# Kernel tuning notes

Measured on AMD Instinct MI355X. Metric: run time of the kernel, lower is better.

Reference implementation:

```python
import jax, jax.numpy as jnp
import numpy as np

EPS = 1e-05
NEG = -1e9

def rotate_half(x):
    x1, x2 = jnp.split(x, 2, axis=-1)
    return jnp.concatenate([-x2, x1], axis=-1)

def rmsnorm(x, w):
    xf = x.astype(jnp.float32)
    n = xf * jax.lax.rsqrt(jnp.mean(xf * xf, axis=-1, keepdims=True) + EPS)
    return w * n.astype(x.dtype)

def setup_inputs() -> dict:
    key = jax.random.key(0)
    ks = jax.random.split(key, 12)
    B, S, H, NH, DH, FF = 1, 2048, 2048, 16, 128, 8192
    x = jax.random.normal(ks[0], (B, S, H), jnp.float32)
    # additive causal mask [1,1,S,S]
    causal = jnp.where(jnp.tril(jnp.ones((S, S), bool)), 0.0, NEG).astype(jnp.float32)
    attention_mask = causal[None, None]
    alibi = 0.1 * jax.random.normal(ks[1], (1, NH, S, S), jnp.float32)
    # rotary angles [S, DH]
    inv = 1.0 / (10000.0 ** (jnp.arange(0, DH, 2, dtype=jnp.float32) / DH))
    ang = jnp.arange(S, dtype=jnp.float32)[:, None] * inv[None, :]
    freqs = jnp.concatenate([ang, ang], axis=-1)  # [S, DH]
    sc = 1.0 / np.sqrt(H)
    wq = sc * jax.random.normal(ks[2], (H, H), jnp.float32)
    wk = sc * jax.random.normal(ks[3], (H, H), jnp.float32)
    wv = sc * jax.random.normal(ks[4], (H, H), jnp.float32)
    wo = sc * jax.random.normal(ks[5], (H, H), jnp.float32)
    w1 = sc * jax.random.normal(ks[6], (H, FF), jnp.float32)
    w3 = sc * jax.random.normal(ks[7], (H, FF), jnp.float32)
    w2 = (1.0 / np.sqrt(FF)) * jax.random.normal(ks[8], (FF, H), jnp.float32)
    attn_norm_w = jnp.ones((H,), jnp.float32)
    ffn_norm_w = jnp.ones((H,), jnp.float32)
    return dict(x=x, attention_mask=attention_mask, alibi=alibi, freqs=freqs,
                wq=wq, wk=wk, wv=wv, wo=wo, w1=w1, w2=w2, w3=w3,
                attn_norm_w=attn_norm_w, ffn_norm_w=ffn_norm_w)

def reference(x, attention_mask, alibi, freqs, wq, wk, wv, wo, w1, w2, w3,
              attn_norm_w, ffn_norm_w):
    B, S, H = x.shape
    NH = 16
    DH = H // NH
    nx = rmsnorm(x, attn_norm_w)
    # projections -> [B, NH, S, DH]
    def heads(y):
        return y.reshape(B, S, NH, DH).transpose(0, 2, 1, 3)
    q = heads(nx @ wq)
    k = heads(nx @ wk)
    v = heads(nx @ wv)
    cos, sin = jnp.cos(freqs), jnp.sin(freqs)  # [S, DH] broadcasts over B,NH
    q = q * cos + rotate_half(q) * sin
    k = k * cos + rotate_half(k) * sin
    scores = jnp.einsum('bhqd,bhkd->bhqk', q, k) / np.sqrt(DH)
    scores = scores + attention_mask + alibi
    attn = jax.nn.softmax(scores, axis=-1)
    out = jnp.einsum('bhqk,bhkd->bhqd', attn, v)
    out = out.transpose(0, 2, 1, 3).reshape(B, S, H)
    x = x + out @ wo
    nx = rmsnorm(x, ffn_norm_w)
    ff = (jax.nn.silu(nx @ w1) * (nx @ w3)) @ w2
    return x + ff
```

## Files before the change

### kernel.cpp

```cpp
#include <hip/hip_runtime.h>
#include <hip/hip_bf16.h>
#include <math.h>

typedef __bf16 bf16x8 __attribute__((ext_vector_type(8)));
typedef float  f32x4  __attribute__((ext_vector_type(4)));
typedef unsigned short u16x8 __attribute__((ext_vector_type(8)));
typedef unsigned short u16x4 __attribute__((ext_vector_type(4)));

#define DEV static __device__ __forceinline__

DEV void gload16(const void* g, void* l) {
  __builtin_amdgcn_global_load_lds((__attribute__((address_space(1))) void*)g,
                                   (__attribute__((address_space(3))) void*)l,
                                   16, 0, 0);
}

DEV float bf2f(unsigned short u) {
  unsigned v = ((unsigned)u) << 16;
  return __builtin_bit_cast(float, v);
}
DEV unsigned short f2bf(float f) {
  unsigned u = __builtin_bit_cast(unsigned, f);
  u = u + 0x7fffu + ((u >> 16) & 1u);
  return (unsigned short)(u >> 16);
}

__global__ __launch_bounds__(256) void rmsnorm_k(const float* __restrict__ x,
    const float* __restrict__ w, unsigned short* __restrict__ out, int H) {
  int row = blockIdx.x;
  const float4* xr = (const float4*)(x + (size_t)row * H);
  float4 a = xr[threadIdx.x * 2], b = xr[threadIdx.x * 2 + 1];
  float ss = a.x*a.x + a.y*a.y + a.z*a.z + a.w*a.w
           + b.x*b.x + b.y*b.y + b.z*b.z + b.w*b.w;
#pragma unroll
  for (int o = 32; o; o >>= 1) ss += __shfl_down(ss, o, 64);
  __shared__ float red[4];
  if ((threadIdx.x & 63) == 0) red[threadIdx.x >> 6] = ss;
  __syncthreads();
  float rs = rsqrtf((red[0] + red[1] + red[2] + red[3]) * (1.0f / 2048.0f) + 1e-5f);
  size_t base = (size_t)row * H + threadIdx.x * 8;
  const float* wv = w + threadIdx.x * 8;
  float vals[8] = {a.x, a.y, a.z, a.w, b.x, b.y, b.z, b.w};
  u16x8 o8;
#pragma unroll
  for (int i = 0; i < 8; ++i) o8[i] = f2bf(vals[i] * rs * wv[i]);
  *(u16x8*)(out + base) = o8;
}

DEV void wtrans_body(const float* __restrict__ W, unsigned short* __restrict__ Wt,
                     int R, int C, int ilv, int bx, int by, int t,
                     unsigned short (*tile)[68]) {
  const int c0 = bx * 64, r0 = by * 64;
  const int lr = t >> 4, lc4 = (t & 15) * 4;
#pragma unroll
  for (int i = 0; i < 4; ++i) {
    float4 v = *(const float4*)&W[(size_t)(r0 + lr + i * 16) * C + c0 + lc4];
    u16x4 s4;
    s4[0] = f2bf(v.x); s4[1] = f2bf(v.y); s4[2] = f2bf(v.z); s4[3] = f2bf(v.w);
    *(u16x4*)&tile[lr + i * 16][lc4] = s4;
  }
  __syncthreads();
  const int oc = t >> 3, seg = (t & 7) * 8;
#pragma unroll
  for (int i = 0; i < 2; ++i) {
    int c = c0 + oc + i * 32;
    u16x8 o8;
#pragma unroll
    for (int j = 0; j < 8; ++j) o8[j] = tile[seg + j][oc + i * 32];
    size_t dstrow = (ilv < 0) ? (size_t)c
                              : (size_t)(c >> 4) * 32 + (c & 15) + ilv * 16;
    *(u16x8*)&Wt[dstrow * R + r0 + seg] = o8;
  }
}

__global__ __launch_bounds__(256) void wtrans64_k(const float* __restrict__ W,
    unsigned short* __restrict__ Wt, int R, int C, int ilv) {
  __shared__ unsigned short tile[64][68];
  wtrans_body(W, Wt, R, C, ilv, blockIdx.x, blockIdx.y, threadIdx.x, tile);
}

__global__ __launch_bounds__(256) void wtrans4_k(
    const float* __restrict__ s0, const float* __restrict__ s1,
    const float* __restrict__ s2, const float* __restrict__ s3,
    unsigned short* __restrict__ d0, unsigned short* __restrict__ d1,
    unsigned short* __restrict__ d2, unsigned short* __restrict__ d3,
    int R, int C) {
  __shared__ unsigned short tile[64][68];
  const float* s = (blockIdx.z == 0) ? s0 : (blockIdx.z == 1) ? s1
                 : (blockIdx.z == 2) ? s2 : s3;
  unsigned short* d = (blockIdx.z == 0) ? d0 : (blockIdx.z == 1) ? d1
                    : (blockIdx.z == 2) ? d2 : d3;
  wtrans_body(s, d, R, C, -1, blockIdx.x, blockIdx.y, threadIdx.x, tile);
}

__global__ __launch_bounds__(256) void wtrans13_k(
    const float* __restrict__ w1, const float* __restrict__ w3,
    unsigned short* __restrict__ dst, int R, int C) {
  __shared__ unsigned short tile[64][68];
  const float* s = blockIdx.z ? w3 : w1;
  wtrans_body(s, dst, R, C, (int)blockIdx.z, blockIdx.x, blockIdx.y,
              threadIdx.x, tile);
}

#define STG_A(H, BUF, KC) do {                                                 \
    gload16(Asrc0 + (size_t)(H) * 128 * lda + (KC),                            \
            &lds[(BUF) * 16384 + (H) * 8192 + w * 1024]);                      \
    gload16(Asrc1 + (size_t)(H) * 128 * lda + (KC),                            \
            &lds[(BUF) * 16384 + (H) * 8192 + w * 1024 + 512]);                \
  } while (0)

#define STG_B(H, BUF, KC) do {                                                 \
    gload16(Bsrc0 + (size_t)(H) * 128 * ldb + (KC),                            \
            &lds[32768 + (BUF) * 16384 + (H) * 8192 + w * 1024]);              \
    gload16(Bsrc1 + (size_t)(H) * 128 * ldb + (KC),                            \
            &lds[32768 + (BUF) * 16384 + (H) * 8192 + w * 1024 + 512]);        \
  } while (0)

#define DS_A(DST, MH) do {                                                     \
    const int abase = buf * 16384 + (MH) * 8192 + arow * 64;                   \
    _Pragma("unroll") for (int m = 0; m < 4; ++m) {                            \
      DST[m][0] = *(const bf16x8*)&lds[abase + m * 1024 + acol0];              \
      DST[m][1] = *(const bf16x8*)&lds[abase + m * 1024 + acol1];              \
    } } while (0)

#define DS_B(DST, NH) do {                                                     \
    const int bbase = 32768 + buf * 16384 + (NH) * 8192 + brow * 64;           \
    _Pragma("unroll") for (int n = 0; n < 2; ++n) {                            \
      DST[n][0] = *(const bf16x8*)&lds[bbase + n * 1024 + acol0];              \
      DST[n][1] = *(const bf16x8*)&lds[bbase + n * 1024 + acol1];              \
    } } while (0)

#define MFMA16(AI, AR, BR) do {                                                \
    _Pragma("unroll") for (int m = 0; m < 4; ++m)                              \
      _Pragma("unroll") for (int n = 0; n < 2; ++n) {                          \
        acc[AI][m][n] = __builtin_amdgcn_mfma_f32_16x16x32_bf16(               \
            AR[m][0], BR[n][0], acc[AI][m][n], 0, 0, 0);                       \
        acc[AI][m][n] = __builtin_amdgcn_mfma_f32_16x16x32_bf16(               \
            AR[m][1], BR[n][1], acc[AI][m][n], 0, 0, 0);                       \
      }                                                                        \
  } while (0)

template <int EPI>
__global__ __launch_bounds__(512, 2) void gemm256_k(
    const unsigned short* __restrict__ A, int lda,
    const unsigned short* __restrict__ B, int ldb,
    unsigned short* __restrict__ Cb, float* __restrict__ Cf,
    int M, int N, int Kext) {
  __shared__ unsigned short lds[65536];
  const int t = threadIdx.x, w = t >> 6, lane = t & 63;
  const int nbm = M >> 8, nbn = N >> 8, nwg = nbm * nbn;
  int id = blockIdx.x;
  id = (id & 7) * (nwg >> 3) + (id >> 3);
  const int bm = id % nbm, bn = id / nbm;
  const size_t m0 = (size_t)bm << 8, n0 = (size_t)bn << 8;
  const int koff = blockIdx.y * Kext;
  const int NT = Kext >> 6;
  const int scol = ((lane & 7) ^ (lane >> 3)) * 8;
  const unsigned short* Asrc0 = A + (m0 + w * 16 + (lane >> 3)) * (size_t)lda + koff + scol;
  const unsigned short* Asrc1 = A + (m0 + w * 16 + 8 + (lane >> 3)) * (size_t)lda + koff + scol;
  const unsigned short* Bsrc0 = B + (n0 + w * 16 + (lane >> 3)) * (size_t)ldb + koff + scol;
  const unsigned short* Bsrc1 = B + (n0 + w * 16 + 8 + (lane >> 3)) * (size_t)ldb + koff + scol;
  const int arow = (w >> 2) * 64 + (lane & 15);
  const int brow = (w & 3) * 32 + (lane & 15);
  const int acol0 = ((lane >> 4) * 8) ^ ((lane & 7) << 3);
  const int acol1 = acol0 ^ 32;
  f32x4 acc[4][4][2] = {};
  bf16x8 Acur[4][2], B0r[2][2], B1r[2][2];
  STG_A(0, 0, 0); STG_B(0, 0, 0); STG_A(1, 0, 0); STG_B(1, 0, 0);
  STG_A(0, 1, 64); STG_B(0, 1, 64);
  asm volatile("s_waitcnt vmcnt(4)" ::: "memory");
  __builtin_amdgcn_s_barrier();
  for (int kt = 0; kt < NT; ++kt) {
    const int buf = kt & 1;
    const int kc1 = (kt + 1) * 64, kc2 = (kt + 2) * 64;
    const bool p1 = (kt + 1 < NT), p2 = (kt + 2 < NT);
    DS_A(Acur, 0); DS_B(B0r, 0); DS_B(B1r, 1);
    if (p1) { STG_A(1, buf ^ 1, kc1); STG_B(1, buf ^ 1, kc1); }
    __builtin_amdgcn_sched_barrier(0);
    __builtin_amdgcn_s_barrier();
    __builtin_amdgcn_s_setprio(1);
    MFMA16(0, Acur, B0r);
    MFMA16(1, Acur, B1r);
    __builtin_amdgcn_s_setprio(0);
    __builtin_amdgcn_sched_barrier(0);
    __builtin_amdgcn_s_barrier();
    DS_A(Acur, 1);
    if (p2) { STG_A(0, buf, kc2); STG_B(0, buf, kc2); }
    __builtin_amdgcn_sched_barrier(0);
    __builtin_amdgcn_s_barrier();
    __builtin_amdgcn_s_setprio(1);
    MFMA16(2, Acur, B0r);
    MFMA16(3, Acur, B1r);
    __builtin_amdgcn_s_setprio(0);
    __builtin_amdgcn_sched_barrier(0);
    if (p2) { asm volatile("s_waitcnt vmcnt(4)" ::: "memory"); }
    else    { asm volatile("s_waitcnt vmcnt(0)" ::: "memory"); }
    __builtin_amdgcn_s_barrier();
  }
#pragma unroll
  for (int Mh = 0; Mh < 2; ++Mh)
#pragma unroll
    for (int Nh = 0; Nh < 2; ++Nh)
#pragma unroll
      for (int m = 0; m < 4; ++m) {
        size_t gr = m0 + Mh * 128 + (w >> 2) * 64 + m * 16 + (lane >> 4) * 4;
        if constexpr (EPI == 2) {
          size_t gc = (n0 >> 1) + Nh * 64 + (w & 3) * 16 + (lane & 15);
          f32x4 v0 = acc[Mh * 2 + Nh][m][0];
          f32x4 v1 = acc[Mh * 2 + Nh][m][1];
#pragma unroll
          for (int j = 0; j < 4; ++j) {
            float s = v0[j] / (1.0f + __expf(-v0[j]));
            Cb[(gr + j) * (size_t)(N >> 1) + gc] = f2bf(s * v1[j]);
          }
        } else {
#pragma unroll
          for (int n = 0; n < 2; ++n) {
            size_t gc = n0 + Nh * 128 + (w & 3) * 32 + n * 16 + (lane & 15);
            f32x4 v = acc[Mh * 2 + Nh][m][n];
#pragma unroll
            for (int j = 0; j < 4; ++j) {
              size_t o = (gr + j) * (size_t)N + gc;
              if constexpr (EPI == 0) Cb[o] = f2bf(v[j]);
              else Cf[(size_t)blockIdx.y * M * N + o] = v[j];
            }
          }
        }
      }
}

template <int EPI>
__global__ __launch_bounds__(256) void gemm_bt_k(
    const unsigned short* __restrict__ A, const unsigned short* __restrict__ B,
    float* __restrict__ Cf, unsigned short* __restrict__ Cb,
    const float* __restrict__ resid, int M, int N, int K) {
  constexpr int BK = 64;
  __shared__ unsigned short lA[128 * BK];
  __shared__ unsigned short lB[128 * BK];
  const int t = threadIdx.x, wave = t >> 6, lane = t & 63;
  int nwg = gridDim.x * gridDim.y;
  int id = blockIdx.y * gridDim.x + blockIdx.x;
  id = (id & 7) * (nwg >> 3) + (id >> 3);
  const int m0 = (id % gridDim.x) * 128, n0 = (id / gridDim.x) * 128;
  const int wr = (wave >> 1) * 64, wc = (wave & 1) * 64;
  f32x4 acc[4][4] = {};
  const int sr = t >> 3;
  const int sc = ((t & 7) ^ (sr & 7)) * 8;
  const unsigned short* Ab = A + (size_t)(m0 + sr) * K + sc;
  const unsigned short* Bb = B + (size_t)(n0 + sr) * K + sc;
  unsigned short* lAw = &lA[(wave * 8) * BK];
  unsigned short* lBw = &lB[(wave * 8) * BK];
  const int row = lane & 15, kg = (lane >> 4) * 8, swz = (lane & 7) << 3;
  for (int k0 = 0; k0 < K; k0 += BK) {
#pragma unroll
    for (int it = 0; it < 4; ++it) {
      gload16(Ab + (size_t)it * 32 * K + k0, lAw + it * 32 * BK);
      gload16(Bb + (size_t)it * 32 * K + k0, lBw + it * 32 * BK);
    }
    asm volatile("s_waitcnt vmcnt(0)" ::: "memory");
    __syncthreads();
#pragma unroll
    for (int kk = 0; kk < 2; ++kk) {
      bf16x8 af[4], bfr[4];
#pragma unroll
      for (int m = 0; m < 4; ++m)
        af[m] = *(const bf16x8*)&lA[(wr + m * 16 + row) * BK + ((kk * 32 + kg) ^ swz)];
#pragma unroll
      for (int n = 0; n < 4; ++n)
        bfr[n] = *(const bf16x8*)&lB[(wc + n * 16 + row) * BK + ((kk * 32 + kg) ^ swz)];
#pragma unroll
      for (int m = 0; m < 4; ++m)
#pragma unroll
        for (int n = 0; n < 4; ++n)
          acc[m][n] = __builtin_amdgcn_mfma_f32_16x16x32_bf16(af[m], bfr[n], acc[m][n], 0, 0, 0);
    }
    __syncthreads();
  }
  const int cg = lane >> 4, col = lane & 15;
#pragma unroll
  for (int m = 0; m < 4; ++m)
#pragma unroll
    for (int n = 0; n < 4; ++n) {
      int rr = m0 + wr + m * 16 + cg * 4;
      int cc = n0 + wc + n * 16 + col;
#pragma unroll
      for (int j = 0; j < 4; ++j) {
        float v = acc[m][n][j];
        size_t o = (size_t)(rr + j) * N + cc;
        if constexpr (EPI == 2) Cf[o] = v + resid[o];
        else if constexpr (EPI == 1) Cf[o] = v;
        else Cb[o] = f2bf(v);
      }
    }
}

__global__ __launch_bounds__(256) void rope_k(const unsigned short* __restrict__ qkv,
    const float* __restrict__ freqs, unsigned short* __restrict__ Qr,
    unsigned short* __restrict__ Kr, int S) {
  int idx = blockIdx.x * 256 + threadIdx.x;
  int dp = idx & 63, h = (idx >> 6) & 15, s = idx >> 10;
  float ang = freqs[s * 128 + dp];
  float c, sn;
  sincosf(ang, &sn, &c);
  size_t rq = (size_t)s * 6144 + h * 128 + dp;
  float q1 = bf2f(qkv[rq]),        q2 = bf2f(qkv[rq + 64]);
  float k1 = bf2f(qkv[rq + 2048]), k2 = bf2f(qkv[rq + 2048 + 64]);
  size_t ob = ((size_t)h * S + s) * 128 + dp;
  Qr[ob]      = f2bf(q1 * c - q2 * sn);
  Qr[ob + 64] = f2bf(q2 * c + q1 * sn);
  Kr[ob]      = f2bf(k1 * c - k2 * sn);
  Kr[ob + 64] = f2bf(k2 * c + k1 * sn);
}

__global__ __launch_bounds__(256) void vtrans_k(const unsigned short* __restrict__ qkv,
    unsigned short* __restrict__ Vt, int S) {
  __shared__ unsigned short tile[32][33];
  int h = blockIdx.z;
  int s0 = blockIdx.x * 32, d0 = blockIdx.y * 32;
  int tx = threadIdx.x, ty = threadIdx.y;
#pragma unroll
  for (int i = 0; i < 4; ++i)
    tile[ty + i * 8][tx] = qkv[(size_t)(s0 + ty + i * 8) * 6144 + 4096 + h * 128 + d0 + tx];
  __syncthreads();
#pragma unroll
  for (int i = 0; i < 4; ++i)
    Vt[((size_t)h * 128 + d0 + ty + i * 8) * S + s0 + tx] = tile[tx][ty + i * 8];
}

#define STGKV(KT, BUF) do {                                                    \
    _Pragma("unroll") for (int it = 0; it < 4; ++it)                           \
      gload16(Kb + (size_t)((KT) * 64 + it * 16 + sr) * 128 + scw,             \
              &lds[(BUF) * 8192 + (it * 16 + wave * 4) * 128]);                \
    _Pragma("unroll") for (int it = 0; it < 4; ++it)                           \
      gload16(Vb + (size_t)(it * 32 + vr) * S + (KT) * 64 + vcw,               \
              &lds[16384 + (BUF) * 8192 + (it * 32 + wave * 8) * 64]);         \
  } while (0)

#define ATTN_TILE(CUR, NXT, KT) do {                                           \
    const int buf = (KT) & 1;                                                  \
    const bool p1 = ((KT) + 1 < ktiles);                                       \
    if (p1) {                                                                  \
      STGKV((KT) + 1, buf ^ 1);                                                \
      _Pragma("unroll") for (int q8 = 0; q8 < 16; ++q8)                        \
        NXT[q8] = albase[(size_t)(q8 & 3) * S + ((KT) + 1) * 64 + (q8 >> 2) * 16]; \
      asm volatile("s_waitcnt vmcnt(24)" ::: "memory");                        \
    } else {                                                                   \
      asm volatile("s_waitcnt vmcnt(0)" ::: "memory");                         \
    }                                                                          \
    __builtin_amdgcn_s_barrier();                                              \
    f32x4 sf[4] = {};                                                          \
    _Pragma("unroll") for (int ks = 0; ks < 4; ++ks)                           \
      _Pragma("unroll") for (int n = 0; n < 4; ++n) {                          \
        bf16x8 kf = *(const bf16x8*)&lds[buf * 8192 + (n * 16 + row) * 128 +   \
                                         ((ks * 32 + kg) ^ kswz)];             \
        sf[n] = __builtin_amdgcn_mfma_f32_16x16x32_bf16(qf[ks], kf, sf[n], 0, 0, 0); \
      }                                                                        \
    float pv[4][4];                                                            \
    float tmax[4] = {-1e30f, -1e30f, -1e30f, -1e30f};                          \
    _Pragma("unroll") for (int n = 0; n < 4; ++n) {                            \
      int k_abs = (KT) * 64 + n * 16 + col;                                    \
      _Pragma("unroll") for (int j = 0; j < 4; ++j) {                          \
        int q_abs = q0 + wave * 16 + cg * 4 + j;                               \
        float v = sf[n][j] * scale + CUR[n * 4 + j];                           \
        if (k_abs > q_abs) v = -1e30f;                                         \
        pv[n][j] = v;                                                          \
        tmax[j] = fmaxf(tmax[j], v);                                           \
      } }                                                                      \
    _Pragma("unroll") for (int o2 = 1; o2 < 16; o2 <<= 1)                      \
      _Pragma("unroll") for (int j = 0; j < 4; ++j)                            \
        tmax[j] = fmaxf(tmax[j], __shfl_xor(tmax[j], o2, 64));                 \
    float alpha[4], rsum[4] = {};                                              \
    _Pragma("unroll") for (int j = 0; j < 4; ++j) {                            \
      float mn = fmaxf(m_run[j], tmax[j]);                                     \
      alpha[j] = __expf(m_run[j] - mn);                                        \
      m_run[j] = mn;                                                           \
    }                                                                          \
    _Pragma("unroll") for (int n = 0; n < 4; ++n)                              \
      _Pragma("unroll") for (int j = 0; j < 4; ++j) {                          \
        float p = __expf(pv[n][j] - m_run[j]);                                 \
        pv[n][j] = p;                                                          \
        rsum[j] += p;                                                          \
      }                                                                        \
    _Pragma("unroll") for (int o2 = 1; o2 < 16; o2 <<= 1)                      \
      _Pragma("unroll") for (int j = 0; j < 4; ++j)                            \
        rsum[j] += __shfl_xor(rsum[j], o2, 64);                                \
    _Pragma("unroll") for (int j = 0; j < 4; ++j)                              \
      l_run[j] = l_run[j] * alpha[j] + rsum[j];                                \
    _Pragma("unroll") for (int nn = 0; nn < 8; ++nn)                           \
      _Pragma("unroll") for (int j = 0; j < 4; ++j) o[nn][j] *= alpha[j];      \
    _Pragma("unroll") for (int n = 0; n < 4; ++n)                              \
      _Pragma("unroll") for (int j = 0; j < 4; ++j) {                          \
        int pr = cg * 4 + j;                                                   \
        pw[pr * 64 + ((n * 16 + col) ^ ((pr & 7) << 3))] = f2bf(pv[n][j]);     \
      }                                                                        \
    asm volatile("s_waitcnt lgkmcnt(0)" ::: "memory");                         \
    __builtin_amdgcn_sched_barrier(0);                                         \
    _Pragma("unroll") for (int kk = 0; kk < 2; ++kk) {                         \
      bf16x8 pf = *(const bf16x8*)&pw[row * 64 + ((kk * 32 + kg) ^ kswz)];     \
      _Pragma("unroll") for (int nn = 0; nn < 8; ++nn) {                       \
        bf16x8 vf = *(const bf16x8*)&lds[16384 + buf * 8192 +                  \
                                         (nn * 16 + row) * 64 +                \
                                         ((kk * 32 + kg) ^ kswz)];             \
        o[nn] = __builtin_amdgcn_mfma_f32_16x16x32_bf16(pf, vf, o[nn], 0, 0, 0); \
      } }                                                                      \
    __builtin_amdgcn_s_barrier();                                              \
  } while (0)

__global__ __launch_bounds__(256) void attn_k(
    const unsigned short* __restrict__ Qr, const unsigned short* __restrict__ Kr,
    const unsigned short* __restrict__ Vt, const float* __restrict__ alibi,
    unsigned short* __restrict__ Ao, int S) {
  __shared__ unsigned short lds[36864];
  const int t = threadIdx.x, wave = t >> 6, lane = t & 63;
  const int h = blockIdx.y, nq = gridDim.x, bx = blockIdx.x;
  const int qt = (bx & 1) ? (nq - 1 - (bx >> 1)) : (bx >> 1);
  const int q0 = qt * 64;
  const int sr = t >> 4, scw = ((t & 15) ^ ((t >> 4) & 7)) * 8;
  const int vr = t >> 3, vcw = ((t & 7) ^ ((t >> 3) & 7)) * 8;
  const unsigned short* Kb = Kr + (size_t)h * S * 128;
  const unsigned short* Vb = Vt + (size_t)h * 128 * S;
  const int row = lane & 15, kg = (lane >> 4) * 8, cg = lane >> 4, col = lane & 15;
  const int kswz = (lane & 7) << 3;
  bf16x8 qf[4];
  const unsigned short* Qrow = Qr + ((size_t)h * S + q0 + wave * 16 + row) * 128;
#pragma unroll
  for (int ks = 0; ks < 4; ++ks) qf[ks] = *(const bf16x8*)&Qrow[ks * 32 + kg];
  f32x4 o[8] = {};
  float m_run[4] = {-1e30f, -1e30f, -1e30f, -1e30f};
  float l_run[4] = {};
  unsigned short* pw = &lds[32768 + wave * 1024];
  const float scale = 0.08838834764831843f;
  const int ktiles = qt + 1;
  const float* albase = alibi + (size_t)h * S * S +
                        ((size_t)q0 + wave * 16 + cg * 4) * S + col;
  float alA[16], alB[16];
  STGKV(0, 0);
#pragma unroll
  for (int q8 = 0; q8 < 16; ++q8)
    alA[q8] = albase[(size_t)(q8 & 3) * S + (q8 >> 2) * 16];
  for (int kt = 0; kt < ktiles; kt += 2) {
    ATTN_TILE(alA, alB, kt);
    if (kt + 1 < ktiles) ATTN_TILE(alB, alA, kt + 1);
  }
#pragma unroll
  for (int nn = 0; nn < 8; ++nn)
#pragma unroll
    for (int j = 0; j < 4; ++j) {
      int q_abs = q0 + wave * 16 + cg * 4 + j;
      Ao[(size_t)q_abs * 2048 + h * 128 + nn * 16 + col] = f2bf(o[nn][j] / l_run[j]);
    }
}

__global__ __launch_bounds__(256) void reduce4_k(const float* __restrict__ part,
    const float* __restrict__ resid, float* __restrict__ out, int n4, size_t mn) {
  int i = blockIdx.x * 256 + threadIdx.x;
  if (i >= n4) return;
  const float4* p = (const float4*)part;
  size_t q = mn >> 2;
  float4 a = ((const float4*)resid)[i];
  float4 s0 = p[i], s1 = p[i + q], s2 = p[i + 2 * q], s3 = p[i + 3 * q];
  float4 r;
  r.x = a.x + s0.x + s1.x + s2.x + s3.x;
  r.y = a.y + s0.y + s1.y + s2.y + s3.y;
  r.z = a.z + s0.z + s1.z + s2.z + s3.z;
  r.w = a.w + s0.w + s1.w + s2.w + s3.w;
  ((float4*)out)[i] = r;
}

extern "C" void kernel_launch(void* const* d_in, const int* in_sizes, int n_in,
                              void* d_out, int out_size, void* d_ws, size_t ws_size,
                              hipStream_t stream) {
  const int S = 2048, H = 2048, NH = 16, DH = 128, FF = 8192;
  const float* x     = (const float*)d_in[0];
  const float* alibi = (const float*)d_in[2];
  const float* freqs = (const float*)d_in[3];
  const float* wq    = (const float*)d_in[4];
  const float* wk    = (const float*)d_in[5];
  const float* wv    = (const float*)d_in[6];
  const float* wo    = (const float*)d_in[7];
  const float* w1    = (const float*)d_in[8];
  const float* w2    = (const float*)d_in[9];
  const float* w3    = (const float*)d_in[10];
  const float* anw   = (const float*)d_in[11];
  const float* fnw   = (const float*)d_in[12];
  float* out = (float*)d_out;

  char* ws = (char*)d_ws;
  size_t off = 0;
  auto alloc = [&](size_t n) { char* p = ws + off; off += (n + 255) & ~(size_t)255; return p; };
  unsigned short* qkvT = (unsigned short*)alloc((size_t)3 * H * H * 2);
  unsigned short* woT  = (unsigned short*)alloc((size_t)H * H * 2);
  unsigned short* w13T = (unsigned short*)alloc((size_t)2 * FF * H * 2);
  unsigned short* w2T  = (unsigned short*)alloc((size_t)H * FF * 2);
  float*          x2   = (float*)alloc((size_t)S * H * 4);
  unsigned short* nx2  = (unsigned short*)alloc((size_t)S * H * 2);
  unsigned short* gbuf = (unsigned short*)alloc((size_t)S * FF * 2);
  unsigned short* nx   = (unsigned short*)alloc((size_t)S * H * 2);
  unsigned short* qkvb = (unsigned short*)alloc((size_t)S * 3 * H * 2);
  unsigned short* Qr   = (unsigned short*)alloc((size_t)NH * S * DH * 2);
  unsigned short* Kr   = (unsigned short*)alloc((size_t)NH * S * DH * 2);
  unsigned short* Vt   = (unsigned short*)alloc((size_t)NH * DH * S * 2);
  unsigned short* attno= (unsigned short*)alloc((size_t)S * H * 2);
  float* part = (float*)ws;

  dim3 tb32(32, 8);
  wtrans4_k<<<dim3(32, 32, 4), 256, 0, stream>>>(
      wq, wk, wv, wo,
      qkvT, qkvT + (size_t)H * H, qkvT + (size_t)2 * H * H, woT, H, H);
  wtrans13_k<<<dim3(128, 32, 2), 256, 0, stream>>>(w1, w3, w13T, H, FF);
  wtrans64_k<<<dim3(32, 128), 256, 0, stream>>>(w2, w2T, FF, H, -1);

  rmsnorm_k<<<S, 256, 0, stream>>>(x, anw, nx, H);
  gemm256_k<0><<<dim3(192, 1), 512, 0, stream>>>(nx, H, qkvT, H, qkvb, nullptr, S, 3 * H, H);
  rope_k<<<(S * NH * 64) / 256, 256, 0, stream>>>(qkvb, freqs, Qr, Kr, S);
  vtrans_k<<<dim3(S / 32, DH / 32, NH), tb32, 0, stream>>>(qkvb, Vt, S);
  attn_k<<<dim3(S / 64, NH), 256, 0, stream>>>(Qr, Kr, Vt, alibi, attno, S);
  gemm_bt_k<2><<<dim3(16, 16), 256, 0, stream>>>(attno, woT, x2, nullptr, x, S, H, H);
  rmsnorm_k<<<S, 256, 0, stream>>>(x2, fnw, nx2, H);
  gemm256_k<2><<<dim3(512, 1), 512, 0, stream>>>(nx2, H, w13T, H, gbuf, nullptr, S, 2 * FF, H);
  gemm256_k<1><<<dim3(64, 4), 512, 0, stream>>>(gbuf, FF, w2T, FF, nullptr, part, S, H, H);
  reduce4_k<<<4096, 256, 0, stream>>>(part, x2, out, S * H / 4, (size_t)S * H);
}
```

Before: 525.2 us.

## Split-K the output projection and fuse residual reduction with FFN RMSNorm

Replaces the 128x128 gemm_bt_k output projection with the larger-tile gemm256 kernel run as a 4-way split-K into a dedicated partial buffer. A new kernel then sums the four partials with the residual, writes x2, and applies the FFN RMSNorm in the same pass, so the separate rmsnorm launch and its re-read of x2 go away. The cost is extra traffic for the 4xSxH fp32 partials and a larger workspace. The w2 GEMM now reuses the same partial buffer, and its K argument is changed to FF/4, apparently matching a per-split K convention.

Result: faster. 511.8 us (-2.6%).

```diff
diff --git a/kernel.cpp b/kernel.cpp
--- a/kernel.cpp
+++ b/kernel.cpp
@@ -45,6 +45,43 @@
 #pragma unroll
   for (int i = 0; i < 8; ++i) o8[i] = f2bf(vals[i] * rs * wv[i]);
   *(u16x8*)(out + base) = o8;
+}
+
+__global__ __launch_bounds__(256) void reduce4rms_k(const float* __restrict__ part,
+    const float* __restrict__ resid, const float* __restrict__ w,
+    float* __restrict__ x2, unsigned short* __restrict__ nxo, int H, size_t mn) {
+  const int row = blockIdx.x, t = threadIdx.x;
+  size_t base = (size_t)row * H + t * 8;
+  float v[8];
+  {
+    float4 a = ((const float4*)(resid + base))[0];
+    float4 b = ((const float4*)(resid + base))[1];
+    v[0]=a.x; v[1]=a.y; v[2]=a.z; v[3]=a.w; v[4]=b.x; v[5]=b.y; v[6]=b.z; v[7]=b.w;
+  }
+#pragma unroll
+  for (int s = 0; s < 4; ++s) {
+    const float4* p4 = (const float4*)(part + (size_t)s * mn + base);
+    float4 pa = p4[0], pb = p4[1];
+    v[0]+=pa.x; v[1]+=pa.y; v[2]+=pa.z; v[3]+=pa.w;
+    v[4]+=pb.x; v[5]+=pb.y; v[6]+=pb.z; v[7]+=pb.w;
+  }
+  float ss = 0.f;
+#pragma unroll
+  for (int i = 0; i < 8; ++i) ss += v[i] * v[i];
+  float4 o0 = {v[0],v[1],v[2],v[3]}, o1 = {v[4],v[5],v[6],v[7]};
+  ((float4*)(x2 + base))[0] = o0;
+  ((float4*)(x2 + base))[1] = o1;
+#pragma unroll
+  for (int o = 32; o; o >>= 1) ss += __shfl_down(ss, o, 64);
+  __shared__ float red[4];
+  if ((t & 63) == 0) red[t >> 6] = ss;
+  __syncthreads();
+  float rs = rsqrtf((red[0] + red[1] + red[2] + red[3]) * (1.0f / 2048.0f) + 1e-5f);
+  const float* wv = w + t * 8;
+  u16x8 o8;
+#pragma unroll
+  for (int i = 0; i < 8; ++i) o8[i] = f2bf(v[i] * rs * wv[i]);
+  *(u16x8*)(nxo + base) = o8;
 }
 
 DEV void wtrans_body(const float* __restrict__ W, unsigned short* __restrict__ Wt,
@@ -227,71 +264,6 @@
           }
         }
       }
-}
-
-template <int EPI>
-__global__ __launch_bounds__(256) void gemm_bt_k(
-    const unsigned short* __restrict__ A, const unsigned short* __restrict__ B,
-    float* __restrict__ Cf, unsigned short* __restrict__ Cb,
-    const float* __restrict__ resid, int M, int N, int K) {
-  constexpr int BK = 64;
-  __shared__ unsigned short lA[128 * BK];
-  __shared__ unsigned short lB[128 * BK];
-  const int t = threadIdx.x, wave = t >> 6, lane = t & 63;
-  int nwg = gridDim.x * gridDim.y;
-  int id = blockIdx.y * gridDim.x + blockIdx.x;
-  id = (id & 7) * (nwg >> 3) + (id >> 3);
-  const int m0 = (id % gridDim.x) * 128, n0 = (id / gridDim.x) * 128;
-  const int wr = (wave >> 1) * 64, wc = (wave & 1) * 64;
-  f32x4 acc[4][4] = {};
-  const int sr = t >> 3;
-  const int sc = ((t & 7) ^ (sr & 7)) * 8;
-  const unsigned short* Ab = A + (size_t)(m0 + sr) * K + sc;
-  const unsigned short* Bb = B + (size_t)(n0 + sr) * K + sc;
-  unsigned short* lAw = &lA[(wave * 8) * BK];
-  unsigned short* lBw = &lB[(wave * 8) * BK];
-  const int row = lane & 15, kg = (lane >> 4) * 8, swz = (lane & 7) << 3;
-  for (int k0 = 0; k0 < K; k0 += BK) {
-#pragma unroll
-    for (int it = 0; it < 4; ++it) {
-      gload16(Ab + (size_t)it * 32 * K + k0, lAw + it * 32 * BK);
-      gload16(Bb + (size_t)it * 32 * K + k0, lBw + it * 32 * BK);
-    }
-    asm volatile("s_waitcnt vmcnt(0)" ::: "memory");
-    __syncthreads();
-#pragma unroll
-    for (int kk = 0; kk < 2; ++kk) {
-      bf16x8 af[4], bfr[4];
-#pragma unroll
-      for (int m = 0; m < 4; ++m)
-        af[m] = *(const bf16x8*)&lA[(wr + m * 16 + row) * BK + ((kk * 32 + kg) ^ swz)];
-#pragma unroll
-      for (int n = 0; n < 4; ++n)
-        bfr[n] = *(const bf16x8*)&lB[(wc + n * 16 + row) * BK + ((kk * 32 + kg) ^ swz)];
-#pragma unroll
-      for (int m = 0; m < 4; ++m)
-#pragma unroll
-        for (int n = 0; n < 4; ++n)
-          acc[m][n] = __builtin_amdgcn_mfma_f32_16x16x32_bf16(af[m], bfr[n], acc[m][n], 0, 0, 0);
-    }
-    __syncthreads();
-  }
-  const int cg = lane >> 4, col = lane & 15;
-#pragma unroll
-  for (int m = 0; m < 4; ++m)
-#pragma unroll
-    for (int n = 0; n < 4; ++n) {
-      int rr = m0 + wr + m * 16 + cg * 4;
-      int cc = n0 + wc + n * 16 + col;
-#pragma unroll
-      for (int j = 0; j < 4; ++j) {
-        float v = acc[m][n][j];
-        size_t o = (size_t)(rr + j) * N + cc;
-        if constexpr (EPI == 2) Cf[o] = v + resid[o];
-        else if constexpr (EPI == 1) Cf[o] = v;
-        else Cb[o] = f2bf(v);
-      }
-    }
 }
 
 __global__ __launch_bounds__(256) void rope_k(const unsigned short* __restrict__ qkv,
@@ -501,7 +473,7 @@
   unsigned short* Kr   = (unsigned short*)alloc((size_t)NH * S * DH * 2);
   unsigned short* Vt   = (unsigned short*)alloc((size_t)NH * DH * S * 2);
   unsigned short* attno= (unsigned short*)alloc((size_t)S * H * 2);
-  float* part = (float*)ws;
+  float* part4 = (float*)alloc((size_t)4 * S * H * 4);
 
   dim3 tb32(32, 8);
   wtrans4_k<<<dim3(32, 32, 4), 256, 0, stream>>>(
@@ -515,9 +487,9 @@
   rope_k<<<(S * NH * 64) / 256, 256, 0, stream>>>(qkvb, freqs, Qr, Kr, S);
   vtrans_k<<<dim3(S / 32, DH / 32, NH), tb32, 0, stream>>>(qkvb, Vt, S);
   attn_k<<<dim3(S / 64, NH), 256, 0, stream>>>(Qr, Kr, Vt, alibi, attno, S);
-  gemm_bt_k<2><<<dim3(16, 16), 256, 0, stream>>>(attno, woT, x2, nullptr, x, S, H, H);
-  rmsnorm_k<<<S, 256, 0, stream>>>(x2, fnw, nx2, H);
+  gemm256_k<1><<<dim3(64, 4), 512, 0, stream>>>(attno, H, woT, H, nullptr, part4, S, H, 512);
+  reduce4rms_k<<<S, 256, 0, stream>>>(part4, x, fnw, x2, nx2, H, (size_t)S * H);
   gemm256_k<2><<<dim3(512, 1), 512, 0, stream>>>(nx2, H, w13T, H, gbuf, nullptr, S, 2 * FF, H);
-  gemm256_k<1><<<dim3(64, 4), 512, 0, stream>>>(gbuf, FF, w2T, FF, nullptr, part, S, H, H);
-  reduce4_k<<<4096, 256, 0, stream>>>(part, x2, out, S * H / 4, (size_t)S * H);
-}
+  gemm256_k<1><<<dim3(64, 4), 512, 0, stream>>>(gbuf, FF, w2T, FF, nullptr, part4, S, H, FF / 4);
+  reduce4_k<<<4096, 256, 0, stream>>>(part4, x2, out, S * H / 4, (size_t)S * H);
+}
```
